# Kernel optimization log

Hardware: AMD Instinct MI355X
Metric: run time of the kernel (lower is better)

## Reference

```python
import jax, jax.numpy as jnp
import numpy as np

T, B, S, D = 512, 32, 512, 512
EPS = 1e-6  # LayerNorm eps


def _ln(x, g, b):
    m = jnp.mean(x, axis=-1, keepdims=True)
    v = jnp.mean((x - m) ** 2, axis=-1, keepdims=True)
    return g * (x - m) * jax.lax.rsqrt(v + EPS) + b


def setup_inputs() -> dict:
    key = jax.random.key(0)
    ks = jax.random.split(key, 10)
    sc = 1.0 / np.sqrt(D).astype(np.float32)
    return {
        "prev_layer": jax.random.normal(ks[0], (T, B, D), jnp.float32),
        "hidden": jax.random.normal(ks[1], (B, D), jnp.float32),
        "enc_output": jax.random.normal(ks[2], (B, S, D), jnp.float32),
        "memory_length": jax.random.randint(ks[3], (B,), 1, S + 1),
        # nn.Linear weights stored as [in, out] (transposed torch layout)
        "W_in": jax.random.normal(ks[4], (D, 3 * D), jnp.float32) * sc,
        "W_enc": jax.random.normal(ks[5], (D, D), jnp.float32) * sc,
        "W_attn_in": jax.random.normal(ks[6], (D, D), jnp.float32) * sc,
        "W_hidden": jax.random.normal(ks[7], (D, D), jnp.float32) * sc,
        "W_ctx": jax.random.normal(ks[8], (D, D), jnp.float32) * sc,
        # LayerNorm gains/biases (5 LNs)
        "g_pre": jnp.ones((3 * D,), jnp.float32), "b_pre": jnp.zeros((3 * D,), jnp.float32),
        "g_enc": jnp.ones((D,), jnp.float32), "b_enc": jnp.zeros((D,), jnp.float32),
        "g_attn": jnp.ones((D,), jnp.float32), "b_attn": jnp.zeros((D,), jnp.float32),
        "g_h": jnp.ones((D,), jnp.float32), "b_h": jnp.zeros((D,), jnp.float32),
        "g_c": jnp.ones((D,), jnp.float32), "b_c": jnp.zeros((D,), jnp.float32),
    }


def reference(prev_layer, hidden, enc_output, W_in, W_enc, W_attn_in, W_hidden,
              W_ctx, g_pre, b_pre, g_enc, b_enc, g_attn, b_attn, g_h, b_h,
              g_c, b_c, memory_length):
    d = prev_layer.shape[-1]
    sqrt_d = jnp.sqrt(jnp.asarray(d, prev_layer.dtype))
    # dropout is identity in eval mode
    preact = _ln(prev_layer @ W_in, g_pre, b_pre)          # [T,B,3D]
    pctx = _ln(enc_output @ W_enc, g_enc, b_enc)           # [B,S,D]
    z, h_gate, pl_t = jnp.split(preact, 3, axis=-1)
    z = jax.nn.sigmoid(z)
    h_gate = jax.nn.sigmoid(h_gate)

    # SRU-style linear recurrence: s_t = (1-z_t)*s_{t-1} + z_t*pl_t
    def step(h, zp):
        z_t, p_t = zp
        s = (1.0 - z_t) * h + z_t * p_t
        return s, s

    hidden_last, ss = jax.lax.scan(step, hidden, (z, pl_t))  # ss: [T,B,D]

    attn_in = _ln(ss @ W_attn_in, g_attn, b_attn)            # [T,B,D]
    align = jnp.einsum('tbd,bsd->bts', attn_in, pctx)        # [B,T,S]
    mask = jnp.arange(pctx.shape[1])[None, :] < memory_length[:, None]  # [B,S]
    align = jnp.where(mask[:, None, :], align, -jnp.inf)
    av = jax.nn.softmax(align / sqrt_d, axis=-1)             # [B,T,S]
    c = jnp.einsum('bts,bsd->tbd', av, pctx)                 # [T,B,D]
    attn_out = c / sqrt_d

    trans = _ln(ss @ W_hidden, g_h, b_h) + _ln(attn_out @ W_ctx, g_c, b_c)
    out = jnp.tanh(trans)
    out = (1.0 - h_gate) * out + h_gate * prev_layer         # [T,B,D]
    p_attn = jnp.transpose(av, (1, 0, 2))                    # [T,B,S]
    return out, hidden_last, p_attn
```

## Files before the change

### kernel.cpp

```cpp
#include <hip/hip_runtime.h>
#include <hip/hip_bf16.h>
#include <cmath>

#define T_ 512
#define B_ 32
#define S_ 512
#define D_ 512
#define NCH 16
#define CT (T_ / NCH)
static constexpr float LN_EPS = 1e-6f;
static constexpr float RSQRT_D = 0.044194173824159216f;

typedef __attribute__((ext_vector_type(8))) __bf16 bf16x8;
typedef __attribute__((ext_vector_type(4))) float f32x4;

struct __align__(8) bfx4 { __hip_bfloat16 x, y, z, w; };
struct __align__(16) u16x8 { unsigned short h[8]; };

__device__ __forceinline__ void g2l16(const void* g, void* l) {
    __builtin_amdgcn_global_load_lds(
        (const __attribute__((address_space(1))) unsigned int*)g,
        (__attribute__((address_space(3))) unsigned int*)l, 16, 0, 0);
}

__device__ __forceinline__ float xr_sum16(float v) {
    v += __shfl_xor(v, 1); v += __shfl_xor(v, 2);
    v += __shfl_xor(v, 4); v += __shfl_xor(v, 8); return v;
}
__device__ __forceinline__ float xr_max16(float v) {
    v = fmaxf(v, __shfl_xor(v, 1)); v = fmaxf(v, __shfl_xor(v, 2));
    v = fmaxf(v, __shfl_xor(v, 4)); v = fmaxf(v, __shfl_xor(v, 8)); return v;
}

__device__ __forceinline__ float sigmoidf_(float x) {
    return 1.f / (1.f + __expf(-x));
}
__device__ __forceinline__ float sigmoid_fast(float x) {
    return __fdividef(1.f, 1.f + __expf(-x));
}
__device__ __forceinline__ float tanh_fast(float x) {
    return 1.f - __fdividef(2.f, __expf(2.f * x) + 1.f);
}
__device__ __forceinline__ float bfu(unsigned short u) {
    unsigned int v = ((unsigned int)u) << 16;
    return __uint_as_float(v);
}
__device__ __forceinline__ unsigned short f2bu(float f) {
    return __hip_bfloat16_raw(__float2bfloat16(f)).x;
}

__device__ __forceinline__ void g128_body(
    const __hip_bfloat16* __restrict__ A, long ldaE,
    const __hip_bfloat16* __restrict__ Bw,
    __hip_bfloat16* __restrict__ out, long outStrideB,
    float2* __restrict__ part, int partMul, int partBase,
    float scale, int bx, int by)
{
    __shared__ char smem[32768];
    const int m0 = by * 128, n0 = bx * 128;
    const int tid = threadIdx.x, lane = tid & 63, w = tid >> 6;
    const int wm = (w >> 1) * 64, wn = (w & 1) * 64;
    const int srow = lane >> 2, skB = (lane & 3) * 16;
    const int q = lane >> 4, c = lane & 15;

    f32x4 acc[4][4];
#pragma unroll
    for (int i = 0; i < 4; i++)
#pragma unroll
        for (int j = 0; j < 4; j++) acc[i][j] = (f32x4)(0.0f);

    const char* ga0 = (const char*)(A + (long)(m0 + w * 16 + srow) * ldaE) + skB;
    const char* ga1 = (const char*)(A + (long)(m0 + (w + 4) * 16 + srow) * ldaE) + skB;
    const char* gb0 = (const char*)(Bw + (long)(n0 + w * 16 + srow) * 512) + skB;
    const char* gb1 = (const char*)(Bw + (long)(n0 + (w + 4) * 16 + srow) * 512) + skB;
    char* la0 = smem + w * 1024 + lane * 16;
    char* la1 = smem + (w + 4) * 1024 + lane * 16;
    char* lb0 = smem + 8192 + w * 1024 + lane * 16;
    char* lb1 = smem + 8192 + (w + 4) * 1024 + lane * 16;
    const char* Ar = smem + (wm + c) * 64 + q * 16;
    const char* Br = smem + 8192 + (wn + c) * 64 + q * 16;

    g2l16(ga0, la0);
    g2l16(ga1, la1);
    g2l16(gb0, lb0);
    g2l16(gb1, lb1);
    __syncthreads();

#pragma unroll
    for (int kk = 0; kk < 16; kk++) {
        const int cb = (kk & 1) << 14;
        const int nb = cb ^ 16384;
        if (kk < 15) {
            const long kb = (long)(kk + 1) * 64;
            g2l16(ga0 + kb, la0 + nb);
            g2l16(ga1 + kb, la1 + nb);
            g2l16(gb0 + kb, lb0 + nb);
            g2l16(gb1 + kb, lb1 + nb);
        }
        bf16x8 af[4], bfr[4];
#pragma unroll
        for (int i = 0; i < 4; i++) {
            af[i] = *(const bf16x8*)(Ar + cb + i * 1024);
            bfr[i] = *(const bf16x8*)(Br + cb + i * 1024);
        }
#pragma unroll
        for (int i = 0; i < 4; i++)
#pragma unroll
            for (int j = 0; j < 4; j++)
                acc[i][j] = __builtin_amdgcn_mfma_f32_16x16x32_bf16(
                    af[i], bfr[j], acc[i][j], 0, 0, 0);
        __syncthreads();
    }

    if (part) {
        float2* sred = (float2*)smem;
#pragma unroll
        for (int i = 0; i < 4; i++)
#pragma unroll
            for (int r = 0; r < 4; r++) {
                float s = 0.f, qq = 0.f;
#pragma unroll
                for (int j = 0; j < 4; j++) {
                    float v = acc[i][j][r] * scale; s += v; qq += v * v;
                }
                s = xr_sum16(s); qq = xr_sum16(qq);
                if (c == 0) sred[(wm + i * 16 + q * 4 + r) * 2 + (w & 1)] =
                    make_float2(s, qq);
            }
        __syncthreads();
        if ((w & 1) == 0 && c == 0) {
#pragma unroll
            for (int i = 0; i < 4; i++)
#pragma unroll
                for (int r = 0; r < 4; r++) {
                    int row = wm + i * 16 + q * 4 + r;
                    float2 a = sred[row * 2], b2 = sred[row * 2 + 1];
                    part[(long)bx * 16384 + (long)(m0 + row) * partMul + partBase] =
                        make_float2(a.x + b2.x, a.y + b2.y);
                }
        }
        __syncthreads();
    }

    for (int p = 0; p < 2; p++) {
        if ((w >> 1) == p) {
#pragma unroll
            for (int i = 0; i < 4; i++)
#pragma unroll
                for (int j = 0; j < 4; j++)
#pragma unroll
                    for (int r = 0; r < 4; r++) {
                        int row = i * 16 + q * 4 + r;
                        int col = wn + j * 16 + c;
                        ((__hip_bfloat16*)smem)[row * 128 + col] =
                            __float2bfloat16(acc[i][j][r] * scale);
                    }
        }
        __syncthreads();
#pragma unroll
        for (int rnd = 0; rnd < 4; rnd++) {
            int row = rnd * 16 + (tid >> 4);
            int ch = tid & 15;
            uint4 v = *(const uint4*)(smem + row * 256 + ch * 16);
            long grow = m0 + p * 64 + row;
            *(uint4*)((char*)out + grow * outStrideB + (long)n0 * 2 + ch * 16) = v;
        }
        __syncthreads();
    }
}

__global__ __launch_bounds__(256) void g128(
    const __hip_bfloat16* __restrict__ A, long ldaE,
    const __hip_bfloat16* __restrict__ Bw, long bStrideZ,
    __hip_bfloat16* __restrict__ out, long outStrideB,
    float2* __restrict__ part, float scale, int swizzle)
{
    int bx, by, pmul = 1, pbase = 0;
    if (gridDim.z > 1) {
        bx = blockIdx.x; by = blockIdx.y;
        A += (long)blockIdx.z * 512;
        Bw += (long)blockIdx.z * bStrideZ;
        out += (long)blockIdx.z * 512;
        pmul = 32; pbase = blockIdx.z;
    } else if (swizzle) {
        const int nwg = gridDim.x * gridDim.y;
        const int lin = blockIdx.y * gridDim.x + blockIdx.x;
        const int cpx = nwg >> 3;
        const int swz = (lin & 7) * cpx + (lin >> 3);
        bx = swz % gridDim.x; by = swz / gridDim.x;
    } else { bx = blockIdx.x; by = blockIdx.y; }
    g128_body(A, ldaE, Bw, out, outStrideB, part, pmul, pbase, scale, bx, by);
}

__global__ __launch_bounds__(256) void g128e2s(
    const __hip_bfloat16* __restrict__ encb,
    const __hip_bfloat16* __restrict__ WE2,
    __hip_bfloat16* __restrict__ E2, float2* __restrict__ partA,
    const __hip_bfloat16* __restrict__ preb, const float2* __restrict__ stats,
    const float* __restrict__ gpre, const float* __restrict__ bpre,
    float* __restrict__ Ap, float* __restrict__ Bp)
{
    const int bid = blockIdx.x;
    if (bid < 512) {
        int i2 = (bid & 31) * 256 + threadIdx.x;
        int b = i2 >> 8, d = (i2 & 255) * 2;
        int idx = b * 512 + d;
        int ch = bid >> 5;
        float2 gz = *(const float2*)(gpre + d), bz = *(const float2*)(bpre + d);
        float2 gp = *(const float2*)(gpre + 1024 + d);
        float2 bp = *(const float2*)(bpre + 1024 + d);
        float A0 = 1.f, s0 = 0.f, A1 = 1.f, s1 = 0.f;
        for (int t = ch * CT; t < (ch + 1) * CT; t++) {
            long row = (long)t * 32 + b;
            float2 st = stats[row];
            ushort2 zr = *(const ushort2*)(preb + row * 1536 + d);
            ushort2 pr = *(const ushort2*)(preb + row * 1536 + 1024 + d);
            float z0 = sigmoidf_((bfu(zr.x) - st.x) * st.y * gz.x + bz.x);
            float z1 = sigmoidf_((bfu(zr.y) - st.x) * st.y * gz.y + bz.y);
            float p0 = (bfu(pr.x) - st.x) * st.y * gp.x + bp.x;
            float p1 = (bfu(pr.y) - st.x) * st.y * gp.y + bp.y;
            A0 *= (1.f - z0); s0 = (1.f - z0) * s0 + z0 * p0;
            A1 *= (1.f - z1); s1 = (1.f - z1) * s1 + z1 * p1;
        }
        *(float2*)(Ap + ch * 16384 + idx) = make_float2(A0, A1);
        *(float2*)(Bp + ch * 16384 + idx) = make_float2(s0, s1);
        return;
    }
    const int local = bid - 512;
    const int swz = (local & 7) * 128 + (local >> 3);
    g128_body(encb, 512, WE2, E2, 2048, partA, 1, 0, 1.f, swz & 7, swz >> 3);
}

__global__ __launch_bounds__(256) void mfix3(
    const __hip_bfloat16* __restrict__ preb, const float2* __restrict__ stats,
    const float* __restrict__ gpre, const float* __restrict__ bpre,
    const float* __restrict__ sinb, __hip_bfloat16* __restrict__ ssb,
    const __hip_bfloat16* __restrict__ E2,
    __hip_bfloat16* __restrict__ pctxb, __hip_bfloat16* __restrict__ pwT,
    const float2* __restrict__ partA,
    const float* __restrict__ g, const float* __restrict__ bb,
    const float* __restrict__ uv)
{
    __shared__ __hip_bfloat16 t[32][34];
    __shared__ float2 sst[32];
    const int bid = blockIdx.x;
    if (bid < 512) {
        int i2 = (bid & 31) * 256 + threadIdx.x;
        int b = i2 >> 8, d = (i2 & 255) * 2;
        int idx = b * 512 + d;
        int ch = bid >> 5;
        float2 gz = *(const float2*)(gpre + d), bz = *(const float2*)(bpre + d);
        float2 gp = *(const float2*)(gpre + 1024 + d);
        float2 bp = *(const float2*)(bpre + 1024 + d);
        float2 sv = *(const float2*)(sinb + ch * 16384 + idx);
        float s0 = sv.x, s1 = sv.y;
        for (int tt = ch * CT; tt < (ch + 1) * CT; tt++) {
            long row = (long)tt * 32 + b;
            float2 st = stats[row];
            ushort2 zr = *(const ushort2*)(preb + row * 1536 + d);
            ushort2 pr = *(const ushort2*)(preb + row * 1536 + 1024 + d);
            float z0 = sigmoidf_((bfu(zr.x) - st.x) * st.y * gz.x + bz.x);
            float z1 = sigmoidf_((bfu(zr.y) - st.x) * st.y * gz.y + bz.y);
            float p0 = (bfu(pr.x) - st.x) * st.y * gp.x + bp.x;
            float p1 = (bfu(pr.y) - st.x) * st.y * gp.y + bp.y;
            s0 += z0 * (p0 - s0);
            s1 += z1 * (p1 - s1);
            ushort2 o;
            o.x = f2bu(s0); o.y = f2bu(s1);
            *(ushort2*)(ssb + (long)tt * 16384 + idx) = o;
        }
        return;
    }
    const int local = bid - 512;
    const int d0 = (local & 15) * 32;
    const int s0 = ((local >> 4) & 15) * 32;
    const int b = local >> 8;
    if (threadIdx.x < 32) {
        long row = (long)b * 512 + s0 + threadIdx.x;
        float s = 0.f, qq = 0.f;
#pragma unroll
        for (int cb = 0; cb < 4; cb++) {
            float2 v = partA[(long)cb * 16384 + row]; s += v.x; qq += v.y;
        }
        float mn = s * (1.f / 512);
        sst[threadIdx.x] =
            make_float2(mn, rsqrtf(qq * (1.f / 512) - mn * mn + LN_EPS));
    }
    __syncthreads();
    const int tx = threadIdx.x & 31, ty = threadIdx.x >> 5;
    const float gv = g[d0 + tx], bv = bb[d0 + tx];
    const float ud = uv[d0 + tx], vd = uv[512 + d0 + tx];
#pragma unroll
    for (int i = 0; i < 4; i++) {
        int srow = s0 + ty + i * 8;
        long row = (long)b * 512 + srow;
        float2 s = sst[ty + i * 8];
        float pc = __bfloat162float(E2[row * 1024 + d0 + tx]);
        pctxb[row * 512 + d0 + tx] =
            __float2bfloat16((pc - s.x) * s.y * gv + bv);
        float pr = __bfloat162float(E2[row * 1024 + 512 + d0 + tx]);
        t[ty + i * 8][tx] = __float2bfloat16(s.y * pr - s.y * s.x * ud + vd);
    }
    __syncthreads();
#pragma unroll
    for (int i = 0; i < 4; i++)
        pwT[(long)b * 262144 + (long)(d0 + ty + i * 8) * 512 + s0 + tx] =
            t[tx][ty + i * 8];
}

#define RC_BUF 34816
__global__ __launch_bounds__(256, 2) void gemm_attn(
    const __hip_bfloat16* __restrict__ attninC2,
    const __hip_bfloat16* __restrict__ pctxb,
    const float2* __restrict__ partB,
    const float* __restrict__ g_att, const float* __restrict__ b_att,
    const int* __restrict__ mlen,
    float* __restrict__ pattn, __hip_bfloat16* __restrict__ softb)
{
    __shared__ char smem[74240];
    float2* sst = (float2*)(smem + 69632);
    float* gln = (float*)(smem + 69888);
    float* bln = (float*)(smem + 71936);
    const int b = blockIdx.z;
    const long t0 = (long)blockIdx.y * 32;
    const int tid = threadIdx.x, lane = tid & 63, w = tid >> 6;

    if (tid < 32) {
        long grow = (t0 + tid) * 32 + b;
        float s = 0.f, qq = 0.f;
#pragma unroll
        for (int cb = 0; cb < 4; cb++) {
            float2 v = partB[(long)cb * 16384 + grow]; s += v.x; qq += v.y;
        }
        float mn = s * (1.f / 512);
        sst[tid] = make_float2(mn, rsqrtf(qq * (1.f / 512) - mn * mn + LN_EPS));
    }
    gln[tid] = g_att[tid]; gln[256 + tid] = g_att[256 + tid];
    bln[tid] = b_att[tid]; bln[256 + tid] = b_att[256 + tid];

    f32x4 acc[2][8];
#pragma unroll
    for (int m = 0; m < 2; m++)
#pragma unroll
        for (int j = 0; j < 8; j++) acc[m][j] = (f32x4)(0.0f);

    const __hip_bfloat16* A = attninC2 + (long)b * 1024 + t0 * 32768;
    const __hip_bfloat16* Bm = pctxb + (long)b * 262144;
    const char* ga = (const char*)(A + (long)(w * 16 + (lane >> 2)) * 32768) + (lane & 3) * 16;
    char* la = smem + w * 1024 + lane * 16;
    const char* gb = (const char*)(Bm + (long)(w * 128 + (lane >> 2)) * 512) + (lane & 3) * 16;
    char* lb = smem + 2048 + w * 8192 + lane * 16;
    const long ldbB16 = 512L * 32;
    const char* Ar = smem + (lane & 15) * 64 + (lane >> 4) * 16;
    const char* Br = smem + 2048 + (w * 128 + (lane & 15)) * 64 + (lane >> 4) * 16;

    if (w < 2) g2l16(ga, la);
#pragma unroll
    for (int s = 0; s < 8; s++) g2l16(gb + s * ldbB16, lb + s * 1024);
    __syncthreads();

    const int fr = lane & 15, kq = lane >> 4;
    const float2 st0 = sst[fr], st1 = sst[16 + fr];

#pragma unroll
    for (int kk = 0; kk < 16; kk++) {
        const int cb = (kk & 1) * RC_BUF;
        const int nb = ((kk & 1) ^ 1) * RC_BUF;
        if (kk < 15) {
            const long kb = (long)(kk + 1) * 64;
            if (w < 2) g2l16(ga + kb, la + nb);
#pragma unroll
            for (int s = 0; s < 8; s++)
                g2l16(gb + kb + s * ldbB16, lb + nb + s * 1024);
        }
        bf16x8 af[2], bfr[8];
#pragma unroll
        for (int m = 0; m < 2; m++) af[m] = *(const bf16x8*)(Ar + cb + m * 1024);
#pragma unroll
        for (int j = 0; j < 8; j++) bfr[j] = *(const bf16x8*)(Br + cb + j * 1024);
        {
            const int k0 = kk * 32 + kq * 8;
            float4 gq0 = *(const float4*)(gln + k0);
            float4 gq1 = *(const float4*)(gln + k0 + 4);
            float4 bq0 = *(const float4*)(bln + k0);
            float4 bq1 = *(const float4*)(bln + k0 + 4);
            float gj[8] = {gq0.x, gq0.y, gq0.z, gq0.w, gq1.x, gq1.y, gq1.z, gq1.w};
            float bj[8] = {bq0.x, bq0.y, bq0.z, bq0.w, bq1.x, bq1.y, bq1.z, bq1.w};
            u16x8 u0 = __builtin_bit_cast(u16x8, af[0]);
            u16x8 u1 = __builtin_bit_cast(u16x8, af[1]);
#pragma unroll
            for (int j = 0; j < 8; j++) {
                u0.h[j] = f2bu((bfu(u0.h[j]) - st0.x) * st0.y * gj[j] + bj[j]);
                u1.h[j] = f2bu((bfu(u1.h[j]) - st1.x) * st1.y * gj[j] + bj[j]);
            }
            af[0] = __builtin_bit_cast(bf16x8, u0);
            af[1] = __builtin_bit_cast(bf16x8, u1);
        }
#pragma unroll
        for (int m = 0; m < 2; m++)
#pragma unroll
            for (int j = 0; j < 8; j++)
                acc[m][j] = __builtin_amdgcn_mfma_f32_16x16x32_bf16(
                    af[m], bfr[j], acc[m][j], 0, 0, 0);
        __syncthreads();
    }

    const int q = lane >> 4, c = lane & 15;
    const int len = mlen[b];
    float* sred = (float*)smem;

#pragma unroll
    for (int m = 0; m < 2; m++)
#pragma unroll
        for (int r = 0; r < 4; r++) {
            float mx = -INFINITY;
#pragma unroll
            for (int j = 0; j < 8; j++) {
                int col = w * 128 + j * 16 + c;
                float v = acc[m][j][r] * RSQRT_D;
                acc[m][j][r] = v;
                if (col < len) mx = fmaxf(mx, v);
            }
            mx = xr_max16(mx);
            if (c == 0) sred[(m * 16 + q * 4 + r) * 4 + w] = mx;
        }
    __syncthreads();
    float rmax[2][4];
#pragma unroll
    for (int m = 0; m < 2; m++)
#pragma unroll
        for (int r = 0; r < 4; r++) {
            int row = m * 16 + q * 4 + r;
            rmax[m][r] = fmaxf(fmaxf(sred[row * 4], sred[row * 4 + 1]),
                               fmaxf(sred[row * 4 + 2], sred[row * 4 + 3]));
        }
    __syncthreads();
#pragma unroll
    for (int m = 0; m < 2; m++)
#pragma unroll
        for (int r = 0; r < 4; r++) {
            float s = 0.f;
#pragma unroll
            for (int j = 0; j < 8; j++) {
                int col = w * 128 + j * 16 + c;
                float e = (col < len) ? __expf(acc[m][j][r] - rmax[m][r]) : 0.f;
                acc[m][j][r] = e; s += e;
            }
            s = xr_sum16(s);
            if (c == 0) sred[(m * 16 + q * 4 + r) * 4 + w] = s;
        }
    __syncthreads();
    float rinv[2][4];
#pragma unroll
    for (int m = 0; m < 2; m++)
#pragma unroll
        for (int r = 0; r < 4; r++) {
            int row = m * 16 + q * 4 + r;
            rinv[m][r] = 1.f / (sred[row * 4] + sred[row * 4 + 1] +
                                sred[row * 4 + 2] + sred[row * 4 + 3]);
        }
    __syncthreads();

#pragma unroll
    for (int m = 0; m < 2; m++)
#pragma unroll
        for (int j = 0; j < 8; j++)
#pragma unroll
            for (int r = 0; r < 4; r++) {
                int row = m * 16 + q * 4 + r;
                int col = w * 128 + j * 16 + c;
                float p = acc[m][j][r] * rinv[m][r];
                pattn[((t0 + row) * 32 + b) * 512 + col] = p;
                ((__hip_bfloat16*)smem)[row * 512 + col] = __float2bfloat16(p);
            }
    __syncthreads();
#pragma unroll
    for (int rnd = 0; rnd < 8; rnd++) {
        int row = rnd * 4 + w;
        uint4 v = *(const uint4*)(smem + row * 1024 + lane * 16);
        *(uint4*)((char*)softb + ((t0 + row) * 32 + b) * 1024 + lane * 16) = v;
    }
}

__global__ __launch_bounds__(256) void fin_ep(
    const __hip_bfloat16* __restrict__ h2r,
    const __hip_bfloat16* __restrict__ C2,
    const __hip_bfloat16* __restrict__ preb,
    const float2* __restrict__ partC,
    const float2* __restrict__ partH,
    const float2* __restrict__ st_p,
    const float* __restrict__ g_c, const float* __restrict__ b_c,
    const float* __restrict__ g_h, const float* __restrict__ b_h,
    const float* __restrict__ g_pre, const float* __restrict__ b_pre,
    const float* __restrict__ prev, float* __restrict__ out)
{
    __shared__ float2 shc[32], shh[32];
    const long m0 = (long)blockIdx.x * 32;
    const int tid = threadIdx.x;
    if (tid < 32) {
        long rowg = m0 + tid;
        float s = 0.f, qq = 0.f;
#pragma unroll
        for (int cb = 0; cb < 4; cb++) {
            float2 v = partC[(long)cb * 16384 + rowg]; s += v.x; qq += v.y;
        }
        float mn = s * (1.f / 512);
        shc[tid] = make_float2(mn, rsqrtf(qq * (1.f / 512) - mn * mn + LN_EPS));
    } else if (tid < 64) {
        long rowg = m0 + tid - 32;
        float s = 0.f, qq = 0.f;
#pragma unroll
        for (int cb = 0; cb < 4; cb++) {
            float2 v = partH[(long)cb * 16384 + rowg]; s += v.x; qq += v.y;
        }
        float mn = s * (1.f / 512);
        shh[tid - 32] = make_float2(mn, rsqrtf(qq * (1.f / 512) - mn * mn + LN_EPS));
    }
    __syncthreads();
#pragma unroll
    for (int ch = 0; ch < 16; ch++) {
        int f4 = ch * 256 + tid;
        int row = f4 >> 7;
        long rowg = m0 + row;
        int col = (f4 & 127) * 4;
        ushort4 h2 = *(const ushort4*)((const char*)h2r + rowg * 1024 + col * 2);
        ushort4 h1 = *(const ushort4*)((const char*)C2 + rowg * 2048 + 1024 + col * 2);
        ushort4 hr = *(const ushort4*)((const char*)preb + rowg * 3072 + 1024 + col * 2);
        float4 pv = *(const float4*)(prev + rowg * 512 + col);
        float4 gc = *(const float4*)(g_c + col), bc = *(const float4*)(b_c + col);
        float4 gh = *(const float4*)(g_h + col), bh = *(const float4*)(b_h + col);
        float4 gp = *(const float4*)(g_pre + 512 + col);
        float4 bp = *(const float4*)(b_pre + 512 + col);
        float2 sc = shc[row], sh = shh[row], sp = st_p[rowg];
        auto fuse = [&](unsigned short h2u, unsigned short h1u, unsigned short hru,
                        float pvv, float gcv, float bcv, float ghv, float bhv,
                        float gpv, float bpv) -> float {
            float t2 = (bfu(h2u) - sc.x) * sc.y * gcv + bcv;
            float t1 = (bfu(h1u) - sh.x) * sh.y * ghv + bhv;
            float hg = sigmoid_fast((bfu(hru) - sp.x) * sp.y * gpv + bpv);
            return (1.f - hg) * tanh_fast(t1 + t2) + hg * pvv;
        };
        float4 o;
        o.x = fuse(h2.x, h1.x, hr.x, pv.x, gc.x, bc.x, gh.x, bh.x, gp.x, bp.x);
        o.y = fuse(h2.y, h1.y, hr.y, pv.y, gc.y, bc.y, gh.y, bh.y, gp.y, bp.y);
        o.z = fuse(h2.z, h1.z, hr.z, pv.z, gc.z, bc.z, gh.z, bh.z, gp.z, bp.z);
        o.w = fuse(h2.w, h1.w, hr.w, pv.w, gc.w, bc.w, gh.w, bh.w, gp.w, bp.w);
        *(float4*)(out + rowg * 512 + col) = o;
    }
}

__global__ __launch_bounds__(256) void cvt4(
    const float* __restrict__ x, __hip_bfloat16* __restrict__ y, int n4)
{
    int i = blockIdx.x * 256 + threadIdx.x;
    if (i >= n4) return;
    float4 v = ((const float4*)x)[i];
    bfx4 o;
    o.x = __float2bfloat16(v.x); o.y = __float2bfloat16(v.y);
    o.z = __float2bfloat16(v.z); o.w = __float2bfloat16(v.w);
    ((bfx4*)y)[i] = o;
}

__global__ __launch_bounds__(256) void wtrans(
    const float* __restrict__ w0, const float* __restrict__ w1,
    const float* __restrict__ w2, const float* __restrict__ w3,
    const float* __restrict__ w4, __hip_bfloat16* __restrict__ WT,
    __hip_bfloat16* __restrict__ WE2)
{
    int z = blockIdx.z;
    const float* W; __hip_bfloat16* O; int N;
    if (z == 0)      { W = w0; O = WT;                          N = 1536; }
    else if (z == 1) { W = w1; O = WE2;                         N = 512; }
    else if (z == 2) { W = w2; O = WT + 786432 + 262144;        N = 512; }
    else if (z == 3) { W = w3; O = WT + 786432 + 524288;        N = 512; }
    else             { W = w4; O = WT + 786432 + 786432;        N = 512; }
    int n0 = blockIdx.x * 32, k0 = blockIdx.y * 32;
    if (n0 >= N) return;
    __shared__ float t[32][33];
    int tx = threadIdx.x & 31, ty = threadIdx.x >> 5;
#pragma unroll
    for (int i = 0; i < 4; i++)
        t[ty + i * 8][tx] = W[(long)(k0 + ty + i * 8) * N + n0 + tx];
    __syncthreads();
#pragma unroll
    for (int i = 0; i < 4; i++)
        O[(long)(n0 + ty + i * 8) * 512 + k0 + tx] =
            __float2bfloat16(t[tx][ty + i * 8]);
}

__global__ __launch_bounds__(256) void wgscale(
    const __hip_bfloat16* __restrict__ wctxT, const float* __restrict__ g,
    __hip_bfloat16* __restrict__ wgT)
{
    int i = blockIdx.x * 256 + threadIdx.x;
    int d1 = i & 511;
    wgT[i] = __float2bfloat16(__bfloat162float(wctxT[i]) * g[d1]);
}

__global__ __launch_bounds__(256) void uvk(
    const float* __restrict__ Wctx, const float* __restrict__ g,
    const float* __restrict__ b, float* __restrict__ uv)
{
    int d = blockIdx.x * 256 + threadIdx.x;
    float u = 0.f, v = 0.f;
    for (int k = 0; k < 512; k++) {
        float w = Wctx[(long)k * 512 + d];
        u += g[k] * w; v += b[k] * w;
    }
    uv[d] = u; uv[512 + d] = v;
}

__global__ __launch_bounds__(256) void stats_fin(
    const float2* __restrict__ part, float2* __restrict__ stats)
{
    int r = blockIdx.x * 256 + threadIdx.x;
    float s = 0.f, qq = 0.f;
#pragma unroll
    for (int cb = 0; cb < 12; cb++) {
        float2 v = part[(long)cb * 16384 + r]; s += v.x; qq += v.y;
    }
    float m = s * (1.f / 1536);
    float rs = rsqrtf(qq * (1.f / 1536) - m * m + LN_EPS);
    stats[r] = make_float2(m, rs);
}

__global__ __launch_bounds__(256) void scan_part2(
    const float* __restrict__ Ap, const float* __restrict__ Bp,
    const float* __restrict__ h0, float* __restrict__ sin_,
    float* __restrict__ hlast)
{
    int idx = blockIdx.x * 256 + threadIdx.x;
    float s = h0[idx];
    for (int ch = 0; ch < NCH; ch++) {
        sin_[ch * 16384 + idx] = s;
        s = Ap[ch * 16384 + idx] * s + Bp[ch * 16384 + idx];
    }
    hlast[idx] = s;
}

extern "C" void kernel_launch(void* const* d_in, const int* in_sizes, int n_in,
                              void* d_out, int out_size, void* d_ws, size_t ws_size,
                              hipStream_t stream) {
    const float* prev  = (const float*)d_in[0];
    const float* hid0  = (const float*)d_in[1];
    const float* enc   = (const float*)d_in[2];
    const int*   mlen  = (const int*)  d_in[3];
    const float* W_in  = (const float*)d_in[4];
    const float* W_enc = (const float*)d_in[5];
    const float* W_att = (const float*)d_in[6];
    const float* W_hid = (const float*)d_in[7];
    const float* W_ctx = (const float*)d_in[8];
    const float* g_pre = (const float*)d_in[9];
    const float* b_pre = (const float*)d_in[10];
    const float* g_enc = (const float*)d_in[11];
    const float* b_enc = (const float*)d_in[12];
    const float* g_att = (const float*)d_in[13];
    const float* b_att = (const float*)d_in[14];
    const float* g_h   = (const float*)d_in[15];
    const float* b_h   = (const float*)d_in[16];
    const float* g_c   = (const float*)d_in[17];
    const float* b_c   = (const float*)d_in[18];

    float* out   = (float*)d_out;
    float* hlast = out + (long)T_ * B_ * D_;
    float* pattn = hlast + (long)B_ * D_;

    char* ws = (char*)d_ws;
    __hip_bfloat16* preb    = (__hip_bfloat16*)(ws);
    __hip_bfloat16* WT      = (__hip_bfloat16*)(ws + 50331648);
    __hip_bfloat16* prevb   = (__hip_bfloat16*)(ws + 54525952);
    __hip_bfloat16* encb    = (__hip_bfloat16*)(ws + 71303168);
    __hip_bfloat16* pctxb   = (__hip_bfloat16*)(ws + 88080384);
    __hip_bfloat16* pwT     = (__hip_bfloat16*)(ws + 104857600);
    __hip_bfloat16* ssb     = (__hip_bfloat16*)(ws + 121634816);
    __hip_bfloat16* C2      = (__hip_bfloat16*)(ws + 138412032);
    __hip_bfloat16* E2      = (__hip_bfloat16*)(ws + 171966464);
    __hip_bfloat16* softb   = (__hip_bfloat16*)(ws + 171966464);
    __hip_bfloat16* h2raw   = (__hip_bfloat16*)(ws + 188743680);
    float2* part            = (float2*)(ws + 205520896);
    float2* stats           = (float2*)(ws + 207618048);
    float* scanA            = (float*)(ws + 207749120);
    float* scanB            = (float*)(ws + 208797696);
    float* sinb             = (float*)(ws + 209846272);
    __hip_bfloat16* WE2     = (__hip_bfloat16*)(ws + 211419136);
    float* uv               = (float*)(ws + 212467712);
    __hip_bfloat16* WgT     = (__hip_bfloat16*)scanA;
    __hip_bfloat16* Wencbf  = (__hip_bfloat16*)scanB;

    float2* partA = part;
    float2* partB = part + 8 * 16384;
    float2* partC = part;

    const __hip_bfloat16* W_attT = WT + 786432 + 262144;
    const __hip_bfloat16* W_ctxT = WT + 786432 + 786432;

    dim3 blk(256);

    cvt4<<<8192, blk, 0, stream>>>(prev, prevb, 2097152);
    cvt4<<<8192, blk, 0, stream>>>(enc, encb, 2097152);
    cvt4<<<256, blk, 0, stream>>>(W_enc, Wencbf, 65536);
    wtrans<<<dim3(48, 16, 5), blk, 0, stream>>>(W_in, W_enc, W_att, W_hid,
                                                W_ctx, WT, WE2);
    wgscale<<<1024, blk, 0, stream>>>(W_ctxT, g_enc, WgT);
    uvk<<<2, blk, 0, stream>>>(W_ctx, g_enc, b_enc, uv);
    g128<<<dim3(4, 4), blk, 0, stream>>>(WgT, 512, Wencbf, 0, WE2 + 262144,
                                         1024, nullptr, 1.f, 0);

    g128<<<dim3(12, 128), blk, 0, stream>>>(prevb, 512, WT, 0, preb, 3072,
                                            part, 1.f, 1);
    stats_fin<<<64, blk, 0, stream>>>(part, stats);

    g128e2s<<<1536, blk, 0, stream>>>(encb, WE2, E2, partA, preb, stats,
                                      g_pre, b_pre, scanA, scanB);
    scan_part2<<<64, blk, 0, stream>>>(scanA, scanB, hid0, sinb, hlast);

    mfix3<<<8704, blk, 0, stream>>>(preb, stats, g_pre, b_pre, sinb, ssb,
                                    E2, pctxb, pwT, partA, g_enc, b_enc, uv);

    g128<<<dim3(8, 128), blk, 0, stream>>>(ssb, 512, W_attT, 0, C2, 2048,
                                           partB, 1.f, 1);

    gemm_attn<<<dim3(1, 16, 32), blk, 0, stream>>>(C2, pctxb, partB,
                                                   g_att, b_att, mlen,
                                                   pattn, softb);

    g128<<<dim3(4, 4, 32), blk, 0, stream>>>(softb, 16384, pwT, 262144,
                                             h2raw, 32768, partC, RSQRT_D, 0);

    fin_ep<<<512, blk, 0, stream>>>(h2raw, C2, preb, partC,
                                    partB + 4 * 16384, stats,
                                    g_c, b_c, g_h, b_h, g_pre, b_pre, prev,
                                    out);
}
```

Baseline: 434.6 us.

## Triple-buffer g128 LDS pipeline and merge small prep kernel launches

The shared GEMM body moves from double to triple buffering in LDS, prefetching two K-steps ahead. It replaces the per-iteration __syncthreads with explicit vmcnt waits and raw barriers, so global-to-LDS loads can overlap MFMA work. The input conversion kernels and the weight prep kernels (W_ctx scaling, W_enc conversion, u/v reduction) are merged into fewer launches to cut launch overhead. Raising LDS to 48KB may reduce blocks per CU, and the hand-written waitcnt logic has to stay correct with the number of loads in flight.

```diff
diff --git a/kernel.cpp b/kernel.cpp
--- a/kernel.cpp
+++ b/kernel.cpp
@@ -56,7 +56,7 @@
     float2* __restrict__ part, int partMul, int partBase,
     float scale, int bx, int by)
 {
-    __shared__ char smem[32768];
+    __shared__ char smem[49152];
     const int m0 = by * 128, n0 = bx * 128;
     const int tid = threadIdx.x, lane = tid & 63, w = tid >> 6;
     const int wm = (w >> 1) * 64, wn = (w & 1) * 64;
@@ -84,14 +84,20 @@
     g2l16(ga1, la1);
     g2l16(gb0, lb0);
     g2l16(gb1, lb1);
-    __syncthreads();
+    g2l16(ga0 + 64, la0 + 16384);
+    g2l16(ga1 + 64, la1 + 16384);
+    g2l16(gb0 + 64, lb0 + 16384);
+    g2l16(gb1 + 64, lb1 + 16384);
+    asm volatile("s_waitcnt vmcnt(4)" ::: "memory");
+    __builtin_amdgcn_s_barrier();
+    __builtin_amdgcn_sched_barrier(0);
 
 #pragma unroll
     for (int kk = 0; kk < 16; kk++) {
-        const int cb = (kk & 1) << 14;
-        const int nb = cb ^ 16384;
-        if (kk < 15) {
-            const long kb = (long)(kk + 1) * 64;
+        const int cb = (kk % 3) * 16384;
+        if (kk < 14) {
+            const int nb = ((kk + 2) % 3) * 16384;
+            const long kb = (long)(kk + 2) * 64;
             g2l16(ga0 + kb, la0 + nb);
             g2l16(ga1 + kb, la1 + nb);
             g2l16(gb0 + kb, lb0 + nb);
@@ -109,8 +115,16 @@
             for (int j = 0; j < 4; j++)
                 acc[i][j] = __builtin_amdgcn_mfma_f32_16x16x32_bf16(
                     af[i], bfr[j], acc[i][j], 0, 0, 0);
-        __syncthreads();
-    }
+        if (kk < 15) {
+            if (kk < 14)
+                asm volatile("s_waitcnt vmcnt(4) lgkmcnt(0)" ::: "memory");
+            else
+                asm volatile("s_waitcnt vmcnt(0) lgkmcnt(0)" ::: "memory");
+            __builtin_amdgcn_s_barrier();
+            __builtin_amdgcn_sched_barrier(0);
+        }
+    }
+    __syncthreads();
 
     if (part) {
         float2* sred = (float2*)smem;
@@ -549,16 +563,19 @@
     }
 }
 
-__global__ __launch_bounds__(256) void cvt4(
-    const float* __restrict__ x, __hip_bfloat16* __restrict__ y, int n4)
+__global__ __launch_bounds__(256) void cvt4d(
+    const float* __restrict__ a, __hip_bfloat16* __restrict__ ya,
+    const float* __restrict__ b, __hip_bfloat16* __restrict__ yb)
 {
     int i = blockIdx.x * 256 + threadIdx.x;
-    if (i >= n4) return;
-    float4 v = ((const float4*)x)[i];
+    const float* x; __hip_bfloat16* y; int k;
+    if (i < 2097152) { x = a; y = ya; k = i; }
+    else { x = b; y = yb; k = i - 2097152; }
+    float4 v = ((const float4*)x)[k];
     bfx4 o;
     o.x = __float2bfloat16(v.x); o.y = __float2bfloat16(v.y);
     o.z = __float2bfloat16(v.z); o.w = __float2bfloat16(v.w);
-    ((bfx4*)y)[i] = o;
+    ((bfx4*)y)[k] = o;
 }
 
 __global__ __launch_bounds__(256) void wtrans(
@@ -588,26 +605,34 @@
             __float2bfloat16(t[tx][ty + i * 8]);
 }
 
-__global__ __launch_bounds__(256) void wgscale(
+__global__ __launch_bounds__(256) void wprep(
     const __hip_bfloat16* __restrict__ wctxT, const float* __restrict__ g,
-    __hip_bfloat16* __restrict__ wgT)
-{
-    int i = blockIdx.x * 256 + threadIdx.x;
-    int d1 = i & 511;
-    wgT[i] = __float2bfloat16(__bfloat162float(wctxT[i]) * g[d1]);
-}
-
-__global__ __launch_bounds__(256) void uvk(
-    const float* __restrict__ Wctx, const float* __restrict__ g,
-    const float* __restrict__ b, float* __restrict__ uv)
-{
-    int d = blockIdx.x * 256 + threadIdx.x;
-    float u = 0.f, v = 0.f;
-    for (int k = 0; k < 512; k++) {
-        float w = Wctx[(long)k * 512 + d];
-        u += g[k] * w; v += b[k] * w;
-    }
-    uv[d] = u; uv[512 + d] = v;
+    __hip_bfloat16* __restrict__ wgT,
+    const float* __restrict__ Wenc, __hip_bfloat16* __restrict__ wencb,
+    const float* __restrict__ Wctx, const float* __restrict__ bvec,
+    float* __restrict__ uv)
+{
+    const int bid = blockIdx.x;
+    if (bid < 1024) {
+        int i = bid * 256 + threadIdx.x;
+        int d1 = i & 511;
+        wgT[i] = __float2bfloat16(__bfloat162float(wctxT[i]) * g[d1]);
+    } else if (bid < 1280) {
+        int i = (bid - 1024) * 256 + threadIdx.x;
+        float4 v = ((const float4*)Wenc)[i];
+        bfx4 o;
+        o.x = __float2bfloat16(v.x); o.y = __float2bfloat16(v.y);
+        o.z = __float2bfloat16(v.z); o.w = __float2bfloat16(v.w);
+        ((bfx4*)wencb)[i] = o;
+    } else {
+        int d = (bid - 1280) * 256 + threadIdx.x;
+        float u = 0.f, v = 0.f;
+        for (int k = 0; k < 512; k++) {
+            float w = Wctx[(long)k * 512 + d];
+            u += g[k] * w; v += bvec[k] * w;
+        }
+        uv[d] = u; uv[512 + d] = v;
+    }
 }
 
 __global__ __launch_bounds__(256) void stats_fin(
@@ -696,13 +721,11 @@
 
     dim3 blk(256);
 
-    cvt4<<<8192, blk, 0, stream>>>(prev, prevb, 2097152);
-    cvt4<<<8192, blk, 0, stream>>>(enc, encb, 2097152);
-    cvt4<<<256, blk, 0, stream>>>(W_enc, Wencbf, 65536);
+    cvt4d<<<16384, blk, 0, stream>>>(prev, prevb, enc, encb);
     wtrans<<<dim3(48, 16, 5), blk, 0, stream>>>(W_in, W_enc, W_att, W_hid,
                                                 W_ctx, WT, WE2);
-    wgscale<<<1024, blk, 0, stream>>>(W_ctxT, g_enc, WgT);
-    uvk<<<2, blk, 0, stream>>>(W_ctx, g_enc, b_enc, uv);
+    wprep<<<1282, blk, 0, stream>>>(W_ctxT, g_enc, WgT, W_enc, Wencbf,
+                                    W_ctx, b_enc, uv);
     g128<<<dim3(4, 4), blk, 0, stream>>>(WgT, 512, Wencbf, 0, WE2 + 262144,
                                          1024, nullptr, 1.f, 0);
 
```

New measurement: 488.4 us. +12.4%, slower.
